# Performance work log

Hardware: AMD Instinct MI355X
Metric: run time of the kernel (lower is better)

## Reference

```python
import jax, jax.numpy as jnp
import numpy as np

N_NODES = 50000
N_EDGES = 400000
IN_DIM = 512
OUT_DIM = 128
EPS = 1e-12  # F.normalize eps


def setup_inputs() -> dict:
    key = jax.random.key(0)
    ks = jax.random.split(key, 8)
    x = jax.random.normal(ks[0], (N_NODES, IN_DIM), dtype=jnp.float32)
    edge_index = jax.random.randint(ks[1], (2, N_EDGES), 0, N_NODES, dtype=jnp.int64)
    def glorot(k, fan_in, fan_out):
        s = jnp.sqrt(6.0 / (fan_in + fan_out)).astype(jnp.float32)
        return jax.random.uniform(k, (fan_in, fan_out), jnp.float32, -s, s)
    return {
        "x": x,
        "edge_index": edge_index,
        "W1": glorot(ks[2], IN_DIM, 512), "b1": jnp.zeros((512,), jnp.float32),
        "W2": glorot(ks[3], 512, 256),    "b2": jnp.zeros((256,), jnp.float32),
        "W3": glorot(ks[4], 256, OUT_DIM), "b3": jnp.zeros((OUT_DIM,), jnp.float32),
    }


def _gcn_layer(x, W, b, src, dst, dinv):
    # PyG GCNConv: h = x @ W; propagate with sym-norm D^-1/2 (A+I) D^-1/2; out += bias
    h = x @ W                                   # [N, F_out] dense GEMM (compute core)
    coef = dinv[src] * dinv[dst]                # [E]
    msg = h[src] * coef[:, None]                # gather + scale  [E, F_out]
    agg = jnp.zeros_like(h).at[dst].add(msg)    # scatter-add over destination nodes
    agg = agg + h * (dinv * dinv)[:, None]      # self-loop contribution
    return agg + b


def reference(x, edge_index, W1, b1, W2, b2, W3, b3):
    src, dst = edge_index[0], edge_index[1]
    n = x.shape[0]
    # degree with self-loops: deg[i] = 1 + in-degree(i)
    deg = jnp.ones((n,), x.dtype).at[dst].add(1.0)
    dinv = jax.lax.rsqrt(deg)
    # eval mode: F.dropout(training=False) is identity
    z = jax.nn.relu(_gcn_layer(x, W1, b1, src, dst, dinv))
    z = jax.nn.relu(_gcn_layer(z, W2, b2, src, dst, dinv))
    z = jax.nn.relu(_gcn_layer(z, W3, b3, src, dst, dinv))
    z = z / jnp.sum(z)
    z = jnp.tanh(z) ** 2
    norm = jnp.maximum(jnp.linalg.norm(z, axis=1, keepdims=True), EPS)
    return z / norm
```

## Files before the change

kernel.cpp:

```cpp
#include <hip/hip_runtime.h>
#include <math.h>

#define NN 50000
#define NE 400000
#define SLOTS 32
#define MT2 196
#define BXPG2 25

typedef unsigned short u16;
typedef __bf16 bf16x8 __attribute__((ext_vector_type(8)));
typedef float f32x4 __attribute__((ext_vector_type(4)));
typedef unsigned int u32x4 __attribute__((ext_vector_type(4)));
typedef u16 bfu8 __attribute__((ext_vector_type(8)));
typedef u16 bfu4 __attribute__((ext_vector_type(4)));

__device__ __forceinline__ u16 f2bf(float f) {
    unsigned u = __builtin_bit_cast(unsigned, f);
    u += 0x7fff + ((u >> 16) & 1);
    return (u16)(u >> 16);
}
__device__ __forceinline__ float bf2f(u16 h) {
    unsigned u = ((unsigned)h) << 16;
    return __builtin_bit_cast(float, u);
}

__device__ __forceinline__ void gload_lds16(const void* g, void* l) {
    typedef __attribute__((address_space(1))) const unsigned int GU;
    typedef __attribute__((address_space(3))) unsigned int LU;
    __builtin_amdgcn_global_load_lds((GU*)g, (LU*)l, 16, 0, 0);
}

__global__ void cvt_w(const float* __restrict__ W1, u16* __restrict__ Wt1,
                      const float* __restrict__ W2, u16* __restrict__ Wt2,
                      const float* __restrict__ W3, u16* __restrict__ Wt3) {
    int idx = blockIdx.x * blockDim.x + threadIdx.x;
    if (idx < 262144) {
        int n = idx >> 9, k = idx & 511;
        Wt1[idx] = f2bf(W1[(size_t)k * 512 + n]);
        return;
    }
    idx -= 262144;
    if (idx < 131072) {
        int n = idx >> 9, k = idx & 511;
        Wt2[idx] = f2bf(W2[(size_t)k * 256 + n]);
        return;
    }
    idx -= 131072;
    if (idx < 32768) {
        int n = idx >> 8, k = idx & 255;
        Wt3[idx] = f2bf(W3[(size_t)k * 128 + n]);
    }
}

__global__ void init_ell(int* __restrict__ ell, int* __restrict__ cnt, int N) {
    int i = blockIdx.x * blockDim.x + threadIdx.x;
    const int total4 = N * SLOTS / 4;
    if (i < total4) {
        int4 v = make_int4(N, N, N, N);
        reinterpret_cast<int4*>(ell)[i] = v;
    }
    if (i < N) cnt[i] = 0;
}

__global__ void build_ell(const int* __restrict__ src, const int* __restrict__ dst,
                          int* __restrict__ cnt, int* __restrict__ ell, int E) {
    int e = blockIdx.x * blockDim.x + threadIdx.x;
    if (e < E) {
        const int d = dst[e];
        int pos = atomicAdd(&cnt[d], 1);
        if (pos < SLOTS) ell[d * SLOTS + pos] = src[e];
    }
}

__global__ void make_dinv(const int* __restrict__ cnt, float* __restrict__ dinv, int N) {
    int i = blockIdx.x * blockDim.x + threadIdx.x;
    if (i < N) dinv[i] = rsqrtf(1.0f + (float)cnt[i]);
    if (i == 0) dinv[N] = 0.f;
}

template <int NT, int CVT, int KK>
__global__ __launch_bounds__(512) void gemm_bf16(
    const void* __restrict__ Xv, const u16* __restrict__ Wt,
    u16* __restrict__ H, int N, int NO)
{
    const int k8 = blockIdx.x & 7;
    const int idx = blockIdx.x >> 3;
    const int bx = k8 * BXPG2 + idx / NT;
    const int nt = idx - (idx / NT) * NT;
    const int m0 = bx * 256;
    if (m0 >= N) return;
    const int n0 = nt * 128;

    const u16* X = (const u16*)Xv;
    const float* Xf = (const float*)Xv;

    __shared__ unsigned char lds[CVT ? 81920 : 49152];
    const int tid = threadIdx.x;
    const int w = tid >> 6;
    const int lane = tid & 63;
    const int wr = w >> 1;
    const int wc = w & 1;

    f32x4 acc[4][4] = {};

    const int brow = tid >> 2;
    const int bgcol = (((tid & 3) ^ (brow & 3)) << 3);
    const int bgrow = n0 + brow;

    if constexpr (CVT) {
        const int gcolf = (((tid & 7) ^ ((tid >> 3) & 7)) << 2);
        int agrow4[4];
        #pragma unroll
        for (int i = 0; i < 4; ++i) {
            int rr = m0 + i * 64 + (tid >> 3);
            agrow4[i] = (rr < N) ? rr : N - 1;
        }

        #pragma unroll
        for (int i = 0; i < 4; ++i)
            gload_lds16(Xf + (size_t)agrow4[i] * KK + gcolf,
                        lds + i * 8192 + w * 1024);
        gload_lds16(Wt + (size_t)bgrow * KK + bgcol, lds + 65536 + w * 1024);
        asm volatile("s_waitcnt vmcnt(0)" ::: "memory");
        __syncthreads();

        int cur = 0;
        for (int k0 = 0; k0 < KK; k0 += 32) {
            const bool more = (k0 + 32 < KK);
            if (more) {
                const int na = (cur ^ 1) * 32768;
                const int nb = 65536 + (cur ^ 1) * 8192;
                #pragma unroll
                for (int i = 0; i < 4; ++i)
                    gload_lds16(Xf + (size_t)agrow4[i] * KK + k0 + 32 + gcolf,
                                lds + na + i * 8192 + w * 1024);
                gload_lds16(Wt + (size_t)bgrow * KK + k0 + 32 + bgcol,
                            lds + nb + w * 1024);
            }

            const int ca = cur * 32768;
            const int cbb = 65536 + cur * 8192;
            bf16x8 af[4], bfr[4];
            #pragma unroll
            for (int m = 0; m < 4; ++m) {
                const int r = wr * 64 + m * 16 + (lane & 15);
                const int g = lane >> 4;
                const int j0 = (2 * g) ^ (r & 7);
                const int j1 = (2 * g + 1) ^ (r & 7);
                const f32x4 lo = *reinterpret_cast<const f32x4*>(lds + ca + r * 128 + j0 * 16);
                const f32x4 hi = *reinterpret_cast<const f32x4*>(lds + ca + r * 128 + j1 * 16);
                unsigned q0, q1, q2, q3;
                asm("v_cvt_pk_bf16_f32 %0, %1, %2" : "=v"(q0) : "v"(lo[0]), "v"(lo[1]));
                asm("v_cvt_pk_bf16_f32 %0, %1, %2" : "=v"(q1) : "v"(lo[2]), "v"(lo[3]));
                asm("v_cvt_pk_bf16_f32 %0, %1, %2" : "=v"(q2) : "v"(hi[0]), "v"(hi[1]));
                asm("v_cvt_pk_bf16_f32 %0, %1, %2" : "=v"(q3) : "v"(hi[2]), "v"(hi[3]));
                u32x4 t; t[0] = q0; t[1] = q1; t[2] = q2; t[3] = q3;
                af[m] = __builtin_bit_cast(bf16x8, t);
            }
            #pragma unroll
            for (int n = 0; n < 4; ++n) {
                const int r = wc * 64 + n * 16 + (lane & 15);
                const int off = cbb + r * 64 + (((lane >> 4) ^ (r & 3)) * 16);
                bfr[n] = *reinterpret_cast<const bf16x8*>(lds + off);
            }
            #pragma unroll
            for (int m = 0; m < 4; ++m)
                #pragma unroll
                for (int n = 0; n < 4; ++n)
                    acc[m][n] = __builtin_amdgcn_mfma_f32_16x16x32_bf16(
                        af[m], bfr[n], acc[m][n], 0, 0, 0);

            asm volatile("s_waitcnt vmcnt(0)" ::: "memory");
            __syncthreads();
            cur ^= 1;
        }
    } else {
        const int gcol = (((tid & 3) ^ ((tid >> 2) & 3)) << 3);
        int agrow2[2];
        #pragma unroll
        for (int i = 0; i < 2; ++i) {
            int rr = m0 + i * 128 + (tid >> 2);
            agrow2[i] = (rr < N) ? rr : N - 1;
        }

        #pragma unroll
        for (int i = 0; i < 2; ++i)
            gload_lds16(X + (size_t)agrow2[i] * KK + gcol,
                        lds + i * 8192 + w * 1024);
        gload_lds16(Wt + (size_t)bgrow * KK + bgcol, lds + 32768 + w * 1024);
        asm volatile("s_waitcnt vmcnt(0)" ::: "memory");
        __syncthreads();

        int cur = 0;
        for (int k0 = 0; k0 < KK; k0 += 32) {
            const bool more = (k0 + 32 < KK);
            if (more) {
                const int na = (cur ^ 1) * 16384;
                const int nb = 32768 + (cur ^ 1) * 8192;
                #pragma unroll
                for (int i = 0; i < 2; ++i)
                    gload_lds16(X + (size_t)agrow2[i] * KK + k0 + 32 + gcol,
                                lds + na + i * 8192 + w * 1024);
                gload_lds16(Wt + (size_t)bgrow * KK + k0 + 32 + bgcol,
                            lds + nb + w * 1024);
            }

            const int ca = cur * 16384;
            const int cbb = 32768 + cur * 8192;
            bf16x8 af[4], bfr[4];
            #pragma unroll
            for (int m = 0; m < 4; ++m) {
                const int r = wr * 64 + m * 16 + (lane & 15);
                const int off = ca + r * 64 + (((lane >> 4) ^ (r & 3)) * 16);
                af[m] = *reinterpret_cast<const bf16x8*>(lds + off);
            }
            #pragma unroll
            for (int n = 0; n < 4; ++n) {
                const int r = wc * 64 + n * 16 + (lane & 15);
                const int off = cbb + r * 64 + (((lane >> 4) ^ (r & 3)) * 16);
                bfr[n] = *reinterpret_cast<const bf16x8*>(lds + off);
            }
            #pragma unroll
            for (int m = 0; m < 4; ++m)
                #pragma unroll
                for (int n = 0; n < 4; ++n)
                    acc[m][n] = __builtin_amdgcn_mfma_f32_16x16x32_bf16(
                        af[m], bfr[n], acc[m][n], 0, 0, 0);

            asm volatile("s_waitcnt vmcnt(0)" ::: "memory");
            __syncthreads();
            cur ^= 1;
        }
    }

    float* Cs = reinterpret_cast<float*>(lds);
    #pragma unroll
    for (int rh = 0; rh < 2; ++rh) {
        #pragma unroll
        for (int c = 0; c < 2; ++c) {
            __syncthreads();
            if ((wr >> 1) == rh && wc == c) {
                const int rbase = (wr & 1) * 64;
                #pragma unroll
                for (int m = 0; m < 4; ++m)
                    #pragma unroll
                    for (int n = 0; n < 4; ++n)
                        #pragma unroll
                        for (int r = 0; r < 4; ++r) {
                            int row = rbase + m * 16 + (lane >> 4) * 4 + r;
                            int col = n * 16 + (lane & 15);
                            Cs[row * 66 + col] = acc[m][n][r];
                        }
            }
            __syncthreads();
            const int row = tid >> 2;
            const int q = tid & 3;
            const int grow = m0 + rh * 128 + row;
            if (grow < N) {
                const float* p = Cs + row * 66 + q * 16;
                bfu8 oA, oB;
                #pragma unroll
                for (int j = 0; j < 8; ++j) oA[j] = f2bf(p[j]);
                #pragma unroll
                for (int j = 0; j < 8; ++j) oB[j] = f2bf(p[8 + j]);
                bfu8* dst = reinterpret_cast<bfu8*>(H + (size_t)grow * NO + n0 + c * 64 + q * 16);
                dst[0] = oA; dst[1] = oB;
            }
        }
    }
}

template <int F, int LPN, bool BFOUT, bool SUMOUT>
__global__ __launch_bounds__(128) void aggregate_bf(
    const u16* __restrict__ H, const int* __restrict__ cnt,
    const int* __restrict__ ell, const float* __restrict__ dinv,
    const float* __restrict__ bias, void* __restrict__ Aout,
    float* __restrict__ partials, int N)
{
    constexpr int EPL = F / LPN;
    const int gtid = blockIdx.x * blockDim.x + threadIdx.x;
    const int node = gtid / LPN;
    const int lane = gtid - node * LPN;
    const int co = lane * EPL;
    const bool valid = node < N;

    float a0[EPL], a1[EPL], a2[EPL], a3[EPL];
    #pragma unroll
    for (int q = 0; q < EPL; ++q) { a0[q] = 0.f; a1[q] = 0.f; a2[q] = 0.f; a3[q] = 0.f; }

    if (valid) {
        const int base = node * SLOTS;
        const int c = min(cnt[node], SLOTS);
        const int pd = (c + 3) & ~3;
        for (int j = 0; j < pd; j += 4) {
            const int4 s4 = *reinterpret_cast<const int4*>(ell + base + j);
            const float d0 = dinv[s4.x];
            const float d1 = dinv[s4.y];
            const float d2 = dinv[s4.z];
            const float d3 = dinv[s4.w];
            if constexpr (EPL == 8) {
                bfu8 v0 = *reinterpret_cast<const bfu8*>(H + (size_t)s4.x * F + co);
                bfu8 v1 = *reinterpret_cast<const bfu8*>(H + (size_t)s4.y * F + co);
                bfu8 v2 = *reinterpret_cast<const bfu8*>(H + (size_t)s4.z * F + co);
                bfu8 v3 = *reinterpret_cast<const bfu8*>(H + (size_t)s4.w * F + co);
                #pragma unroll
                for (int q = 0; q < 8; ++q) {
                    a0[q] = fmaf(bf2f(v0[q]), d0, a0[q]);
                    a1[q] = fmaf(bf2f(v1[q]), d1, a1[q]);
                    a2[q] = fmaf(bf2f(v2[q]), d2, a2[q]);
                    a3[q] = fmaf(bf2f(v3[q]), d3, a3[q]);
                }
            } else {
                bfu4 v0 = *reinterpret_cast<const bfu4*>(H + (size_t)s4.x * F + co);
                bfu4 v1 = *reinterpret_cast<const bfu4*>(H + (size_t)s4.y * F + co);
                bfu4 v2 = *reinterpret_cast<const bfu4*>(H + (size_t)s4.z * F + co);
                bfu4 v3 = *reinterpret_cast<const bfu4*>(H + (size_t)s4.w * F + co);
                #pragma unroll
                for (int q = 0; q < EPL; ++q) {
                    a0[q] = fmaf(bf2f(v0[q]), d0, a0[q]);
                    a1[q] = fmaf(bf2f(v1[q]), d1, a1[q]);
                    a2[q] = fmaf(bf2f(v2[q]), d2, a2[q]);
                    a3[q] = fmaf(bf2f(v3[q]), d3, a3[q]);
                }
            }
        }
    }

    float r[EPL];
    #pragma unroll
    for (int q = 0; q < EPL; ++q) r[q] = 0.f;
    if (valid) {
        const float dd = dinv[node], dd2 = dd * dd;
        if constexpr (EPL == 8) {
            bfu8 sv = *reinterpret_cast<const bfu8*>(H + (size_t)node * F + co);
            #pragma unroll
            for (int q = 0; q < 8; ++q)
                r[q] = fmaf((a0[q] + a1[q]) + (a2[q] + a3[q]), dd,
                            fmaf(bf2f(sv[q]), dd2, bias[co + q]));
        } else {
            bfu4 sv = *reinterpret_cast<const bfu4*>(H + (size_t)node * F + co);
            #pragma unroll
            for (int q = 0; q < EPL; ++q)
                r[q] = fmaf((a0[q] + a1[q]) + (a2[q] + a3[q]), dd,
                            fmaf(bf2f(sv[q]), dd2, bias[co + q]));
        }
    }

    if constexpr (BFOUT) {
        if (valid) {
            u16* out = reinterpret_cast<u16*>(Aout) + (size_t)node * F + co;
            if constexpr (EPL == 8) {
                bfu8 o;
                #pragma unroll
                for (int q = 0; q < 8; ++q) o[q] = f2bf(fmaxf(r[q], 0.f));
                *reinterpret_cast<bfu8*>(out) = o;
            } else {
                bfu4 o;
                #pragma unroll
                for (int q = 0; q < EPL; ++q) o[q] = f2bf(fmaxf(r[q], 0.f));
                *reinterpret_cast<bfu4*>(out) = o;
            }
        }
    } else if constexpr (SUMOUT) {
        float ls = 0.f;
        if (valid) {
            float* out = reinterpret_cast<float*>(Aout) + (size_t)node * F + co;
            #pragma unroll
            for (int q = 0; q < EPL; ++q) {
                const float z = fmaxf(r[q], 0.f);
                out[q] = z;
                ls += z;
            }
        }
        const int wl = threadIdx.x & 63, wi = threadIdx.x >> 6;
        #pragma unroll
        for (int off = 32; off; off >>= 1) ls += __shfl_down(ls, off);
        __shared__ float wsum[2];
        if (wl == 0) wsum[wi] = ls;
        __syncthreads();
        if (threadIdx.x == 0)
            partials[blockIdx.x] = wsum[0] + wsum[1];
    } else {
        if (valid) {
            float* out = reinterpret_cast<float*>(Aout) + (size_t)node * F + co;
            #pragma unroll
            for (int q = 0; q < EPL; ++q) out[q] = r[q];
        }
    }
}

__global__ __launch_bounds__(1024) void reduce_partials(const float* __restrict__ partials,
                                                        float* __restrict__ S, int n) {
    float local = 0.f;
    for (int i = threadIdx.x; i < n; i += 1024) local += partials[i];
    const int lane = threadIdx.x & 63, wid = threadIdx.x >> 6;
    #pragma unroll
    for (int off = 32; off; off >>= 1) local += __shfl_down(local, off);
    __shared__ float wsum[16];
    if (lane == 0) wsum[wid] = local;
    __syncthreads();
    if (threadIdx.x == 0) {
        float t = 0.f;
        #pragma unroll
        for (int i = 0; i < 16; ++i) t += wsum[i];
        *S = t;
    }
}

__global__ void final_norm(float* __restrict__ Z, const float* __restrict__ S, int N) {
    const int wid = threadIdx.x >> 6;
    const int lane = threadIdx.x & 63;
    const int row = blockIdx.x * 4 + wid;
    if (row >= N) return;
    const float inv = 1.0f / (*S);
    float v0 = Z[(size_t)row * 128 + lane] * inv;
    float v1 = Z[(size_t)row * 128 + lane + 64] * inv;
    const float t0 = tanhf(v0), t1 = tanhf(v1);
    const float y0 = t0 * t0, y1 = t1 * t1;
    float ss = y0 * y0 + y1 * y1;
    #pragma unroll
    for (int off = 32; off; off >>= 1) ss += __shfl_xor(ss, off);
    const float nrm = fmaxf(sqrtf(ss), 1e-12f);
    const float innrm = 1.0f / nrm;
    Z[(size_t)row * 128 + lane]      = y0 * innrm;
    Z[(size_t)row * 128 + lane + 64] = y1 * innrm;
}

extern "C" void kernel_launch(void* const* d_in, const int* in_sizes, int n_in,
                              void* d_out, int out_size, void* d_ws, size_t ws_size,
                              hipStream_t stream) {
    const float* x  = (const float*)d_in[0];
    const int*   ei = (const int*)d_in[1];
    const float* W1 = (const float*)d_in[2];
    const float* b1 = (const float*)d_in[3];
    const float* W2 = (const float*)d_in[4];
    const float* b2 = (const float*)d_in[5];
    const float* W3 = (const float*)d_in[6];
    const float* b3 = (const float*)d_in[7];
    float* out = (float*)d_out;

    const int N = NN, E = NE;
    const int* src = ei;
    const int* dst = ei + E;

    char* ws = (char*)d_ws;
    size_t off = 0;
    u16* bufA = (u16*)(ws + off); off += (size_t)(N + 1) * 512 * 2;
    u16* bufB = (u16*)(ws + off); off += (size_t)(N + 1) * 512 * 2;
    u16* Wt1 = (u16*)(ws + off); off += 512 * 512 * 2;
    u16* Wt2 = (u16*)(ws + off); off += 256 * 512 * 2;
    u16* Wt3 = (u16*)(ws + off); off += 128 * 256 * 2;
    float* dinv   = (float*)(ws + off); off += 204800;
    int*   cnt    = (int*)  (ws + off); off += 204800;
    float* Ssum   = (float*)(ws + off); off += 256;
    float* partials = (float*)(ws + off); off += 65536;
    int*   ell    = (int*)  (ws + off); off += (size_t)N * SLOTS * 4 + 256;

    cvt_w<<<(262144 + 131072 + 32768 + 255) / 256, 256, 0, stream>>>(
        W1, Wt1, W2, Wt2, W3, Wt3);

    init_ell<<<(N * SLOTS / 4 + 255) / 256, 256, 0, stream>>>(ell, cnt, N);
    build_ell<<<(E + 255) / 256, 256, 0, stream>>>(src, dst, cnt, ell, E);
    make_dinv<<<(N + 255) / 256, 256, 0, stream>>>(cnt, dinv, N);

    gemm_bf16<4, 1, 512><<<8 * BXPG2 * 4, 512, 0, stream>>>(x, Wt1, bufB, N, 512);
    aggregate_bf<512, 64, true, false><<<(N * 64 + 127) / 128, 128, 0, stream>>>(
        bufB, cnt, ell, dinv, b1, bufA, nullptr, N);
    gemm_bf16<2, 0, 512><<<8 * BXPG2 * 2, 512, 0, stream>>>(bufA, Wt2, bufB, N, 256);
    aggregate_bf<256, 32, true, false><<<(N * 32 + 127) / 128, 128, 0, stream>>>(
        bufB, cnt, ell, dinv, b2, bufA, nullptr, N);
    gemm_bf16<1, 0, 256><<<8 * BXPG2 * 1, 512, 0, stream>>>(bufA, Wt3, bufB, N, 128);
    const int aggBlocks3 = (N * 16 + 127) / 128;
    aggregate_bf<128, 16, false, true><<<aggBlocks3, 128, 0, stream>>>(
        bufB, cnt, ell, dinv, b3, out, partials, N);

    reduce_partials<<<1, 1024, 0, stream>>>(partials, Ssum, aggBlocks3);
    final_norm<<<(N + 3) / 4, 256, 0, stream>>>(out, Ssum, N);
}
```

Baseline: 262.0 us.

## Triple-buffer fp32 A tiles in CVT GEMM with partial vmcnt waits

```diff
diff --git a/kernel.cpp b/kernel.cpp
--- a/kernel.cpp
+++ b/kernel.cpp
@@ -83,6 +83,7 @@
     const void* __restrict__ Xv, const u16* __restrict__ Wt,
     u16* __restrict__ H, int N, int NO)
 {
+    constexpr int NK = KK / 32;
     const int k8 = blockIdx.x & 7;
     const int idx = blockIdx.x >> 3;
     const int bx = k8 * BXPG2 + idx / NT;
@@ -94,7 +95,7 @@
     const u16* X = (const u16*)Xv;
     const float* Xf = (const float*)Xv;
 
-    __shared__ unsigned char lds[CVT ? 81920 : 49152];
+    __shared__ unsigned char lds[CVT ? 122880 : 49152];
     const int tid = threadIdx.x;
     const int w = tid >> 6;
     const int lane = tid & 63;
@@ -116,30 +117,30 @@
             agrow4[i] = (rr < N) ? rr : N - 1;
         }
 
-        #pragma unroll
-        for (int i = 0; i < 4; ++i)
-            gload_lds16(Xf + (size_t)agrow4[i] * KK + gcolf,
-                        lds + i * 8192 + w * 1024);
-        gload_lds16(Wt + (size_t)bgrow * KK + bgcol, lds + 65536 + w * 1024);
-        asm volatile("s_waitcnt vmcnt(0)" ::: "memory");
-        __syncthreads();
-
-        int cur = 0;
-        for (int k0 = 0; k0 < KK; k0 += 32) {
-            const bool more = (k0 + 32 < KK);
-            if (more) {
-                const int na = (cur ^ 1) * 32768;
-                const int nb = 65536 + (cur ^ 1) * 8192;
-                #pragma unroll
-                for (int i = 0; i < 4; ++i)
-                    gload_lds16(Xf + (size_t)agrow4[i] * KK + k0 + 32 + gcolf,
-                                lds + na + i * 8192 + w * 1024);
-                gload_lds16(Wt + (size_t)bgrow * KK + k0 + 32 + bgcol,
-                            lds + nb + w * 1024);
-            }
-
-            const int ca = cur * 32768;
-            const int cbb = 65536 + cur * 8192;
+        auto STAGE = [&](int ks, int bi) {
+            const int base = bi * 40960;
+            #pragma unroll
+            for (int i = 0; i < 4; ++i)
+                gload_lds16(Xf + (size_t)agrow4[i] * KK + ks * 32 + gcolf,
+                            lds + base + i * 8192 + w * 1024);
+            gload_lds16(Wt + (size_t)bgrow * KK + ks * 32 + bgcol,
+                        lds + base + 32768 + w * 1024);
+        };
+
+        STAGE(0, 0);
+        if constexpr (NK > 1) STAGE(1, 1);
+        asm volatile("s_waitcnt vmcnt(5)" ::: "memory");
+        __builtin_amdgcn_s_barrier();
+
+        int bi = 0;
+        for (int k = 0; k < NK; ++k) {
+            if (k + 2 < NK) {
+                int nb = bi + 2; if (nb >= 3) nb -= 3;
+                STAGE(k + 2, nb);
+            }
+
+            const int ca = bi * 40960;
+            const int cbb = ca + 32768;
             bf16x8 af[4], bfr[4];
             #pragma unroll
             for (int m = 0; m < 4; ++m) {
@@ -170,9 +171,16 @@
                     acc[m][n] = __builtin_amdgcn_mfma_f32_16x16x32_bf16(
                         af[m], bfr[n], acc[m][n], 0, 0, 0);
 
-            asm volatile("s_waitcnt vmcnt(0)" ::: "memory");
-            __syncthreads();
-            cur ^= 1;
+            __builtin_amdgcn_sched_barrier(0);
+            if (k + 1 < NK) {
+                if (k + 2 < NK) {
+                    asm volatile("s_waitcnt vmcnt(5)" ::: "memory");
+                } else {
+                    asm volatile("s_waitcnt vmcnt(0)" ::: "memory");
+                }
+                __builtin_amdgcn_s_barrier();
+            }
+            ++bi; if (bi >= 3) bi = 0;
         }
     } else {
         const int gcol = (((tid & 3) ^ ((tid >> 2) & 3)) << 3);
```

New measurement: 275.8 us. +5.3%, slower.
